# Performance work log

Measured on AMD Instinct MI355X. Metric: run time of the kernel, lower is better.

Reference implementation:

```python
import jax, jax.numpy as jnp
import numpy as np

N_NODES = 100000
N_EDGES = 1600000
IN_CH, HID_CH, OUT_CH = 128, 128, 64


def gcn_conv(x, edge_index, W, b, n_nodes):
    """PyG-style GCNConv: add self-loops, symmetric deg^-1/2 normalization,
    linear transform, scatter-add aggregation, bias."""
    src, dst = edge_index[0], edge_index[1]
    loop = jnp.arange(n_nodes, dtype=src.dtype)
    src = jnp.concatenate([src, loop])
    dst = jnp.concatenate([dst, loop])
    # degree computed on destination side (includes self-loops)
    deg = jax.ops.segment_sum(jnp.ones_like(dst, dtype=x.dtype), dst,
                              num_segments=n_nodes)
    dinv = jnp.where(deg > 0, jax.lax.rsqrt(deg), jnp.zeros_like(deg))
    norm = dinv[src] * dinv[dst]            # [E+N]
    h = x @ W                               # [N, out] transform before aggregate
    msg = h[src] * norm[:, None]            # [E+N, out] gathered+scaled messages
    out = jax.ops.segment_sum(msg, dst, num_segments=n_nodes)
    return out + b


def setup_inputs() -> dict:
    key = jax.random.key(0)
    ks = jax.random.split(key, 6)
    x = jax.random.normal(ks[0], (N_NODES, IN_CH), dtype=jnp.float32)
    pos_edge_index = jax.random.randint(ks[1], (2, N_EDGES), 0, N_NODES, dtype=jnp.int64)
    neg_edge_index = jax.random.randint(ks[2], (2, N_EDGES), 0, N_NODES, dtype=jnp.int64)
    # Glorot-ish init for weights
    W1 = jax.random.normal(ks[3], (IN_CH, HID_CH), dtype=jnp.float32) / np.sqrt(IN_CH)
    b1 = jnp.zeros((HID_CH,), dtype=jnp.float32)
    W2 = jax.random.normal(ks[4], (HID_CH, OUT_CH), dtype=jnp.float32) / np.sqrt(HID_CH)
    b2 = jnp.zeros((OUT_CH,), dtype=jnp.float32)
    return {"x": x, "pos_edge_index": pos_edge_index,
            "neg_edge_index": neg_edge_index,
            "W1": W1, "b1": b1, "W2": W2, "b2": b2}


def reference(x, pos_edge_index, neg_edge_index, W1, b1, W2, b2):
    n = x.shape[0]
    # encode: conv1 -> relu -> conv2 (message passing uses pos_edge_index)
    h = gcn_conv(x, pos_edge_index, W1, b1, n)
    h = jax.nn.relu(h)
    z = gcn_conv(h, pos_edge_index, W2, b2, n)
    # decode: gather node pairs, elementwise mul, sum over feature dim
    pos_pred = jnp.sum(z[pos_edge_index[0]] * z[pos_edge_index[1]], axis=1)
    neg_pred = jnp.sum(z[neg_edge_index[0]] * z[neg_edge_index[1]], axis=1)
    return (pos_pred, neg_pred)
```

## Files before the change

### kernel.cpp

```cpp
#include <hip/hip_runtime.h>


#define IC1 128
#define OC1 128
#define OC2 64

#define BSH    9
#define BNODES (1 << BSH)
#define NBMAX  512
#define CHB    8192
#define CHH    16384

typedef unsigned int u32;
typedef unsigned short u16;
typedef __attribute__((ext_vector_type(8))) short short8v;
typedef __attribute__((ext_vector_type(4))) float f32x4;

__device__ __forceinline__ u16 f2bf(float f) {
  u32 u = __float_as_uint(f);
  u32 r = (u + 0x7fffu + ((u >> 16) & 1u)) >> 16;
  return (u16)r;
}
__device__ __forceinline__ u32 pack2bf(float lo, float hi) {
  return (u32)f2bf(lo) | ((u32)f2bf(hi) << 16);
}
__device__ __forceinline__ float bflo(u32 w) { return __uint_as_float(w << 16); }
__device__ __forceinline__ float bfhi(u32 w) { return __uint_as_float(w & 0xffff0000u); }

__device__ __forceinline__ int getIdx(const void* p, long long i, int is64) {
  return is64 ? (int)((const long long*)p)[i] : ((const int*)p)[i];
}

__global__ void k_detect(const void* pei, long long E, int n_nodes, int* flagbuf,
                         int* bcnt, int NB) {
  __shared__ int bad;
  if (threadIdx.x == 0) bad = 0;
  __syncthreads();
  long long cnt = E < 4096 ? E : 4096;
  const unsigned long long* p64 = (const unsigned long long*)pei;
  for (long long i = threadIdx.x; i < cnt; i += blockDim.x)
    if (p64[i] >= (unsigned long long)n_nodes) bad = 1;
  for (int i = threadIdx.x; i < NB; i += blockDim.x) bcnt[i] = 0;
  __syncthreads();
  if (threadIdx.x == 0) flagbuf[0] = bad ? 0 : 1;
}

__global__ __launch_bounds__(256) void k_hist(const void* pei, long long E,
                                              const int* flagbuf, int* bcnt, int NB) {
  __shared__ int h[NBMAX];
  int f = flagbuf[0];
  for (int i = threadIdx.x; i < NB; i += 256) h[i] = 0;
  __syncthreads();
  long long e0 = (long long)blockIdx.x * CHH;
  long long e1 = min(E, e0 + CHH);
  for (long long e = e0 + threadIdx.x; e < e1; e += 256)
    atomicAdd(&h[getIdx(pei, E + e, f) >> BSH], 1);
  __syncthreads();
  for (int i = threadIdx.x; i < NB; i += 256)
    if (h[i]) atomicAdd(&bcnt[i], h[i]);
}

__global__ __launch_bounds__(256) void k_scan(const int* bcnt, int* boff,
                                              int* gcur, int* rowst, int NB, int N) {
  __shared__ int sa[256];
  __shared__ int carryS;
  if (threadIdx.x == 0) carryS = 0;
  __syncthreads();
  for (int base = 0; base < NB; base += 256) {
    int i = base + threadIdx.x;
    int v = (i < NB) ? bcnt[i] : 0;
    sa[threadIdx.x] = v;
    __syncthreads();
    for (int off = 1; off < 256; off <<= 1) {
      int t = (threadIdx.x >= off) ? sa[threadIdx.x - off] : 0;
      __syncthreads();
      sa[threadIdx.x] += t;
      __syncthreads();
    }
    int exc = sa[threadIdx.x] - v + carryS;
    if (i < NB) { boff[i] = exc; gcur[i] = exc; }
    __syncthreads();
    if (threadIdx.x == 255) carryS += sa[255];
    __syncthreads();
  }
  if (threadIdx.x == 0) { boff[NB] = carryS; rowst[N] = carryS; }
}

__global__ __launch_bounds__(256) void k_bin(const void* pei, long long E,
                                             const int* flagbuf, int* gcur,
                                             u32* binned, int NB) {
  __shared__ u32 stage[CHB];
  __shared__ int h[NBMAX], lofs[NBMAX + 1], cur[NBMAX], gofs[NBMAX];
  __shared__ int sa[256];
  __shared__ int carryS;
  int f = flagbuf[0];
  int tid = threadIdx.x;
  for (int i = tid; i < NB; i += 256) h[i] = 0;
  if (tid == 0) carryS = 0;
  __syncthreads();
  long long e0 = (long long)blockIdx.x * CHB;
  long long e1 = min(E, e0 + CHB);
  int cc = (int)(e1 - e0);
  for (long long e = e0 + tid; e < e1; e += 256)
    atomicAdd(&h[getIdx(pei, E + e, f) >> BSH], 1);
  __syncthreads();
  for (int base = 0; base < NB; base += 256) {
    int i = base + tid;
    int v = (i < NB) ? h[i] : 0;
    sa[tid] = v;
    __syncthreads();
    for (int off = 1; off < 256; off <<= 1) {
      int t = (tid >= off) ? sa[tid - off] : 0;
      __syncthreads();
      sa[tid] += t;
      __syncthreads();
    }
    int exc = sa[tid] - v + carryS;
    if (i < NB) { lofs[i] = exc; cur[i] = exc; }
    __syncthreads();
    if (tid == 255) carryS += sa[255];
    __syncthreads();
  }
  if (tid == 0) lofs[NB] = cc;
  __syncthreads();
  for (long long e = e0 + tid; e < e1; e += 256) {
    int s = getIdx(pei, e, f);
    int d = getIdx(pei, E + e, f);
    int b = d >> BSH;
    int p = atomicAdd(&cur[b], 1);
    stage[p] = (u32)s | ((u32)(d & (BNODES - 1)) << 20);
  }
  __syncthreads();
  for (int b = tid; b < NB; b += 256) {
    int cnt = cur[b] - lofs[b];
    gofs[b] = cnt ? (atomicAdd(&gcur[b], cnt) - lofs[b]) : 0;
  }
  __syncthreads();
  for (int i = tid; i < cc; i += 256) {
    int lo = 0, hi = NB;
    while (hi - lo > 1) {
      int mid = (lo + hi) >> 1;
      if (lofs[mid] <= i) lo = mid; else hi = mid;
    }
    binned[(long long)i + gofs[lo]] = stage[i];
  }
}

__global__ __launch_bounds__(256) void k_fill2(const u32* __restrict__ binned,
                                               const int* __restrict__ boff,
                                               float* __restrict__ dinv,
                                               int* __restrict__ rowst,
                                               u32* __restrict__ csr, int N) {
  __shared__ int cnt[BNODES], sa[BNODES], sb[BNODES], cursor[BNODES];
  int b = blockIdx.x;
  int v0 = b << BSH;
  int nv = min(BNODES, N - v0);
  int tid = threadIdx.x;
  for (int i = tid; i < BNODES; i += 256) cnt[i] = 0;
  __syncthreads();
  int base = boff[b];
  int j1 = boff[b + 1];
  for (int j = base + tid; j < j1; j += 256)
    atomicAdd(&cnt[binned[j] >> 20], 1);
  __syncthreads();
  for (int i = tid; i < BNODES; i += 256) sa[i] = cnt[i];
  __syncthreads();
  int* A = sa; int* B = sb;
  #pragma unroll 1
  for (int off = 1; off < BNODES; off <<= 1) {
    for (int i = tid; i < BNODES; i += 256)
      B[i] = A[i] + ((i >= off) ? A[i - off] : 0);
    __syncthreads();
    int* t = A; A = B; B = t;
  }
  for (int i = tid; i < nv; i += 256) {
    int c = cnt[i];
    int exc = A[i] - c;
    rowst[v0 + i] = base + exc;
    cursor[i] = exc;
    dinv[v0 + i] = rsqrtf((float)(c + 1));
  }
  __syncthreads();
  for (int j = base + tid; j < j1; j += 256) {
    u32 u = binned[j];
    int p = atomicAdd(&cursor[u >> 20], 1);
    csr[base + p] = u & 0xFFFFFu;
  }
}

__global__ void k_prepw(const float* __restrict__ W, u16* __restrict__ Wt,
                        int OC) {
  int i = blockIdx.x * blockDim.x + threadIdx.x;
  if (i >= 128 * OC) return;
  int k = i / OC, c = i % OC;
  Wt[c * 128 + k] = f2bf(W[i]);
}

template<int OC, bool BF16IN>
__global__ __launch_bounds__(256) void k_gemm_mfma(const void* __restrict__ xin,
                                                   const u16* __restrict__ Wt,
                                                   u16* __restrict__ t, int N) {
  constexpr int CT = OC / 16;
  constexpr int LW = 136;
  __shared__ u16 xs[64][LW];
  __shared__ u16 ws[OC][LW];
  const int tid = threadIdx.x;
  const int lane = tid & 63, wv = tid >> 6;
  const long long rowBase = (long long)blockIdx.x * 64;

  if constexpr (BF16IN) {
    const u16* xg = (const u16*)xin;
    #pragma unroll
    for (int i = tid; i < 64 * 16; i += 256) {
      int r = i >> 4, c = i & 15;
      uint4 v = make_uint4(0u, 0u, 0u, 0u);
      if (rowBase + r < N) v = ((const uint4*)(xg + (rowBase + r) * IC1))[c];
      *(uint4*)&xs[r][c * 8] = v;
    }
  } else {
    const float* xg = (const float*)xin;
    #pragma unroll
    for (int i = tid; i < 64 * 16; i += 256) {
      int r = i >> 4, c = i & 15;
      uint4 o = make_uint4(0u, 0u, 0u, 0u);
      if (rowBase + r < N) {
        const float4* src = (const float4*)(xg + (rowBase + r) * IC1 + c * 8);
        float4 a = src[0], bq = src[1];
        o.x = pack2bf(a.x, a.y);  o.y = pack2bf(a.z, a.w);
        o.z = pack2bf(bq.x, bq.y); o.w = pack2bf(bq.z, bq.w);
      }
      *(uint4*)&xs[r][c * 8] = o;
    }
  }
  #pragma unroll
  for (int i = tid; i < OC * 16; i += 256) {
    int r = i >> 4, c = i & 15;
    *(uint4*)&ws[r][c * 8] = ((const uint4*)(Wt + r * 128))[c];
  }
  __syncthreads();

  const int frow = lane & 15, fk = (lane >> 4) * 8;
  short8v a[4];
  #pragma unroll
  for (int kq = 0; kq < 4; ++kq)
    a[kq] = *(const short8v*)&xs[wv * 16 + frow][kq * 32 + fk];

  f32x4 acc[CT];
  #pragma unroll
  for (int ct = 0; ct < CT; ++ct) {
    acc[ct] = (f32x4){0.f, 0.f, 0.f, 0.f};
    #pragma unroll
    for (int kq = 0; kq < 4; ++kq) {
      short8v bfrag = *(const short8v*)&ws[ct * 16 + frow][kq * 32 + fk];
      acc[ct] = __builtin_amdgcn_mfma_f32_16x16x32_bf16(a[kq], bfrag, acc[ct], 0, 0, 0);
    }
  }

  const int crow0 = (lane >> 4) * 4, ccol = lane & 15;
  #pragma unroll
  for (int ct = 0; ct < CT; ++ct) {
    #pragma unroll
    for (int r = 0; r < 4; ++r) {
      long long row = rowBase + wv * 16 + crow0 + r;
      if (row < N) t[row * OC + ct * 16 + ccol] = f2bf(acc[ct][r]);
    }
  }
}

template<int CH>
__global__ __launch_bounds__(256) void k_agg(const u16* __restrict__ t,
                                             u16* __restrict__ out,
                                             const float* __restrict__ dinv,
                                             const int* __restrict__ rowst,
                                             const u32* __restrict__ csr,
                                             const float* __restrict__ bias,
                                             int N, int relu) {
  constexpr int G   = CH / 8;
  constexpr int EPI = 64 / G;
  long long wid = ((long long)blockIdx.x * blockDim.x + threadIdx.x) >> 6;
  int lane = threadIdx.x & 63;
  if (wid >= N) return;
  int v = (int)wid;
  int sub = lane / G;
  int cl  = lane % G;
  float dv = dinv[v];
  float selfw = (sub == 0) ? dv * dv : 0.f;
  float acc[8];
  {
    uint4 u = ((const uint4*)(t + (long long)v * CH))[cl];
    acc[0] = bflo(u.x) * selfw; acc[1] = bfhi(u.x) * selfw;
    acc[2] = bflo(u.y) * selfw; acc[3] = bfhi(u.y) * selfw;
    acc[4] = bflo(u.z) * selfw; acc[5] = bfhi(u.z) * selfw;
    acc[6] = bflo(u.w) * selfw; acc[7] = bfhi(u.w) * selfw;
  }
  int st = rowst[v];
  int cnt = rowst[v + 1] - st;
  for (int base = 0; base < cnt; base += 64) {
    int m = min(64, cnt - base);
    int s = 0; float w = 0.f;
    if (lane < m) { s = (int)csr[st + base + lane]; w = dinv[s] * dv; }
    int iters = (m + EPI - 1) / EPI;
    #pragma unroll 2
    for (int j = 0; j < iters; ++j) {
      int src  = __shfl(s, j * EPI + sub);
      float ww = __shfl(w, j * EPI + sub);
      uint4 u = ((const uint4*)(t + (long long)src * CH))[cl];
      acc[0] += bflo(u.x) * ww; acc[1] += bfhi(u.x) * ww;
      acc[2] += bflo(u.y) * ww; acc[3] += bfhi(u.y) * ww;
      acc[4] += bflo(u.z) * ww; acc[5] += bfhi(u.z) * ww;
      acc[6] += bflo(u.w) * ww; acc[7] += bfhi(u.w) * ww;
    }
  }
  #pragma unroll
  for (int off = G; off < 64; off <<= 1) {
    #pragma unroll
    for (int i = 0; i < 8; ++i) acc[i] += __shfl_xor(acc[i], off);
  }
  if (sub == 0) {
    float4 b0 = ((const float4*)bias)[cl * 2];
    float4 b1 = ((const float4*)bias)[cl * 2 + 1];
    float o[8] = {acc[0] + b0.x, acc[1] + b0.y, acc[2] + b0.z, acc[3] + b0.w,
                  acc[4] + b1.x, acc[5] + b1.y, acc[6] + b1.z, acc[7] + b1.w};
    if (relu) {
      #pragma unroll
      for (int i = 0; i < 8; ++i) o[i] = fmaxf(o[i], 0.f);
    }
    uint4 w4;
    w4.x = pack2bf(o[0], o[1]); w4.y = pack2bf(o[2], o[3]);
    w4.z = pack2bf(o[4], o[5]); w4.w = pack2bf(o[6], o[7]);
    ((uint4*)(out + (long long)v * CH))[cl] = w4;
  }
}

__global__ __launch_bounds__(256) void k_decode(const u16* __restrict__ z,
                                                const void* pei, const void* nei,
                                                float* __restrict__ out,
                                                long long E, const int* flagbuf) {
  int f = flagbuf[0];
  long long g = ((long long)blockIdx.x * blockDim.x + threadIdx.x) >> 3;
  int wi = threadIdx.x & 7;
  if (g >= 2 * E) return;
  const void* ei = (g < E) ? pei : nei;
  long long e = (g < E) ? g : g - E;
  int s = getIdx(ei, e, f);
  int d = getIdx(ei, E + e, f);
  uint4 a = ((const uint4*)(z + (long long)s * OC2))[wi];
  uint4 b = ((const uint4*)(z + (long long)d * OC2))[wi];
  float p = bflo(a.x) * bflo(b.x) + bfhi(a.x) * bfhi(b.x)
          + bflo(a.y) * bflo(b.y) + bfhi(a.y) * bfhi(b.y)
          + bflo(a.z) * bflo(b.z) + bfhi(a.z) * bfhi(b.z)
          + bflo(a.w) * bflo(b.w) + bfhi(a.w) * bfhi(b.w);
  p += __shfl_xor(p, 4);
  p += __shfl_xor(p, 2);
  p += __shfl_xor(p, 1);
  if (wi == 0) out[g] = p;
}

extern "C" void kernel_launch(void* const* d_in, const int* in_sizes, int n_in,
                              void* d_out, int out_size, void* d_ws, size_t ws_size,
                              hipStream_t stream) {
  const float* x  = (const float*)d_in[0];
  const void*  pei = d_in[1];
  const void*  nei = d_in[2];
  const float* W1 = (const float*)d_in[3];
  const float* b1 = (const float*)d_in[4];
  const float* W2 = (const float*)d_in[5];
  const float* b2 = (const float*)d_in[6];
  float* out = (float*)d_out;

  const int       N  = in_sizes[0] / IC1;
  const long long E  = in_sizes[1] / 2;
  const int       NB = (N + BNODES - 1) >> BSH;

  char* p = (char*)d_ws;
  auto carve = [&](size_t bytes) { char* r = p; p += ((bytes + 255) & ~(size_t)255); return r; };
  int*   flagbuf = (int*)  carve(8);
  float* dinv    = (float*)carve((size_t)N * 4);
  int*   rowst   = (int*)  carve((size_t)(N + 1) * 4);
  int*   bcnt    = (int*)  carve((size_t)NB * 4);
  int*   boff    = (int*)  carve((size_t)(NB + 1) * 4);
  int*   gcur    = (int*)  carve((size_t)NB * 4);
  u32*   binned  = (u32*)  carve((size_t)E * 4);
  u32*   csr     = (u32*)  carve((size_t)E * 4);
  u16*   Wt      = (u16*)  carve((size_t)128 * 128 * 2);
  u16*   bufA    = (u16*)  carve((size_t)N * IC1 * 2);
  u16*   bufB    = (u16*)  carve((size_t)N * IC1 * 2);

  const int B = 256;

  k_detect<<<1, B, 0, stream>>>(pei, E, N, flagbuf, bcnt, NB);
  k_hist<<<dim3((unsigned)((E + CHH - 1) / CHH)), B, 0, stream>>>(pei, E, flagbuf,
                                                                  bcnt, NB);
  k_scan<<<1, B, 0, stream>>>(bcnt, boff, gcur, rowst, NB, N);
  k_bin<<<dim3((unsigned)((E + CHB - 1) / CHB)), B, 0, stream>>>(pei, E, flagbuf,
                                                                 gcur, binned, NB);
  k_fill2<<<dim3(NB), B, 0, stream>>>(binned, boff, dinv, rowst, csr, N);

  k_prepw<<<dim3((128 * OC1 + B - 1) / B), B, 0, stream>>>(W1, Wt, OC1);
  k_gemm_mfma<OC1, false><<<dim3((N + 63) / 64), B, 0, stream>>>(x, Wt, bufA, N);
  k_agg<OC1><<<dim3((N + 3) / 4), B, 0, stream>>>(bufA, bufB, dinv, rowst,
                                                  csr, b1, N, 1);

  k_prepw<<<dim3((128 * OC2 + B - 1) / B), B, 0, stream>>>(W2, Wt, OC2);
  k_gemm_mfma<OC2, true><<<dim3((N + 63) / 64), B, 0, stream>>>(bufB, Wt, bufA, N);
  k_agg<OC2><<<dim3((N + 3) / 4), B, 0, stream>>>(bufA, bufB, dinv, rowst,
                                                  csr, b2, N, 0);

  long long groups = 2 * E;
  dim3 gD((unsigned)((groups * 8 + B - 1) / B));
  k_decode<<<gD, B, 0, stream>>>(bufB, pei, nei, out, E, flagbuf);
}
```

Before: 444.1 us.

## Fold scan into bin/fill kernels, merge weight prep, enlarge GEMM row tiles

Removes the single-block k_scan launch: each k_bin block now recomputes the global bucket prefix from bcnt, and each k_fill2 block sums the preceding bucket counts itself to find its base offset. Weight conversion for both layers is merged into one k_prepw launch. The GEMM now processes 128 rows per block, reads B fragments directly from global instead of staging them in LDS, and reuses each B fragment for two row tiles. It also halves the edge chunk sizes, moves k_fill2 to 512 threads, and unrolls the aggregation loop further. The tradeoff is redundant prefix work in every block and uncached global reads of the weight fragments.

```diff
diff --git a/kernel.cpp b/kernel.cpp
--- a/kernel.cpp
+++ b/kernel.cpp
@@ -8,8 +8,8 @@
 #define BSH    9
 #define BNODES (1 << BSH)
 #define NBMAX  512
-#define CHB    8192
-#define CHH    16384
+#define CHB    4096
+#define CHH    4096
 
 typedef unsigned int u32;
 typedef unsigned short u16;
@@ -32,7 +32,7 @@
 }
 
 __global__ void k_detect(const void* pei, long long E, int n_nodes, int* flagbuf,
-                         int* bcnt, int NB) {
+                         int* bcnt, int* gcur0, int NB) {
   __shared__ int bad;
   if (threadIdx.x == 0) bad = 0;
   __syncthreads();
@@ -40,7 +40,7 @@
   const unsigned long long* p64 = (const unsigned long long*)pei;
   for (long long i = threadIdx.x; i < cnt; i += blockDim.x)
     if (p64[i] >= (unsigned long long)n_nodes) bad = 1;
-  for (int i = threadIdx.x; i < NB; i += blockDim.x) bcnt[i] = 0;
+  for (int i = threadIdx.x; i < NB; i += blockDim.x) { bcnt[i] = 0; gcur0[i] = 0; }
   __syncthreads();
   if (threadIdx.x == 0) flagbuf[0] = bad ? 0 : 1;
 }
@@ -60,37 +60,11 @@
     if (h[i]) atomicAdd(&bcnt[i], h[i]);
 }
 
-__global__ __launch_bounds__(256) void k_scan(const int* bcnt, int* boff,
-                                              int* gcur, int* rowst, int NB, int N) {
-  __shared__ int sa[256];
-  __shared__ int carryS;
-  if (threadIdx.x == 0) carryS = 0;
-  __syncthreads();
-  for (int base = 0; base < NB; base += 256) {
-    int i = base + threadIdx.x;
-    int v = (i < NB) ? bcnt[i] : 0;
-    sa[threadIdx.x] = v;
-    __syncthreads();
-    for (int off = 1; off < 256; off <<= 1) {
-      int t = (threadIdx.x >= off) ? sa[threadIdx.x - off] : 0;
-      __syncthreads();
-      sa[threadIdx.x] += t;
-      __syncthreads();
-    }
-    int exc = sa[threadIdx.x] - v + carryS;
-    if (i < NB) { boff[i] = exc; gcur[i] = exc; }
-    __syncthreads();
-    if (threadIdx.x == 255) carryS += sa[255];
-    __syncthreads();
-  }
-  if (threadIdx.x == 0) { boff[NB] = carryS; rowst[N] = carryS; }
-}
-
 __global__ __launch_bounds__(256) void k_bin(const void* pei, long long E,
-                                             const int* flagbuf, int* gcur,
-                                             u32* binned, int NB) {
+                                             const int* flagbuf, const int* bcnt,
+                                             int* gcur0, u32* binned, int NB) {
   __shared__ u32 stage[CHB];
-  __shared__ int h[NBMAX], lofs[NBMAX + 1], cur[NBMAX], gofs[NBMAX];
+  __shared__ int h[NBMAX], lofs[NBMAX + 1], cur[NBMAX], gofs[NBMAX], gboff[NBMAX];
   __shared__ int sa[256];
   __shared__ int carryS;
   int f = flagbuf[0];
@@ -121,8 +95,25 @@
     if (tid == 255) carryS += sa[255];
     __syncthreads();
   }
-  if (tid == 0) lofs[NB] = cc;
-  __syncthreads();
+  if (tid == 0) { lofs[NB] = cc; carryS = 0; }
+  __syncthreads();
+  for (int base = 0; base < NB; base += 256) {
+    int i = base + tid;
+    int v = (i < NB) ? bcnt[i] : 0;
+    sa[tid] = v;
+    __syncthreads();
+    for (int off = 1; off < 256; off <<= 1) {
+      int t = (tid >= off) ? sa[tid - off] : 0;
+      __syncthreads();
+      sa[tid] += t;
+      __syncthreads();
+    }
+    int exc = sa[tid] - v + carryS;
+    if (i < NB) gboff[i] = exc;
+    __syncthreads();
+    if (tid == 255) carryS += sa[255];
+    __syncthreads();
+  }
   for (long long e = e0 + tid; e < e1; e += 256) {
     int s = getIdx(pei, e, f);
     int d = getIdx(pei, E + e, f);
@@ -133,7 +124,7 @@
   __syncthreads();
   for (int b = tid; b < NB; b += 256) {
     int cnt = cur[b] - lofs[b];
-    gofs[b] = cnt ? (atomicAdd(&gcur[b], cnt) - lofs[b]) : 0;
+    gofs[b] = cnt ? (gboff[b] + atomicAdd(&gcur0[b], cnt) - lofs[b]) : 0;
   }
   __syncthreads();
   for (int i = tid; i < cc; i += 256) {
@@ -146,54 +137,75 @@
   }
 }
 
-__global__ __launch_bounds__(256) void k_fill2(const u32* __restrict__ binned,
-                                               const int* __restrict__ boff,
+__global__ __launch_bounds__(512) void k_fill2(const u32* __restrict__ binned,
+                                               const int* __restrict__ bcnt,
                                                float* __restrict__ dinv,
                                                int* __restrict__ rowst,
-                                               u32* __restrict__ csr, int N) {
+                                               u32* __restrict__ csr, int N, int NB) {
   __shared__ int cnt[BNODES], sa[BNODES], sb[BNODES], cursor[BNODES];
+  __shared__ int redu[8];
+  __shared__ int baseS;
   int b = blockIdx.x;
   int v0 = b << BSH;
   int nv = min(BNODES, N - v0);
   int tid = threadIdx.x;
-  for (int i = tid; i < BNODES; i += 256) cnt[i] = 0;
-  __syncthreads();
-  int base = boff[b];
-  int j1 = boff[b + 1];
-  for (int j = base + tid; j < j1; j += 256)
+  int part = 0;
+  for (int i = tid; i < b; i += 512) part += bcnt[i];
+  #pragma unroll
+  for (int off = 32; off; off >>= 1) part += __shfl_down(part, off);
+  if ((tid & 63) == 0) redu[tid >> 6] = part;
+  for (int i = tid; i < BNODES; i += 512) cnt[i] = 0;
+  __syncthreads();
+  if (tid == 0) {
+    int s = 0;
+    #pragma unroll
+    for (int w = 0; w < 8; ++w) s += redu[w];
+    baseS = s;
+  }
+  __syncthreads();
+  int base = baseS;
+  int j1 = base + bcnt[b];
+  for (int j = base + tid; j < j1; j += 512)
     atomicAdd(&cnt[binned[j] >> 20], 1);
   __syncthreads();
-  for (int i = tid; i < BNODES; i += 256) sa[i] = cnt[i];
+  sa[tid] = cnt[tid];
   __syncthreads();
   int* A = sa; int* B = sb;
   #pragma unroll 1
   for (int off = 1; off < BNODES; off <<= 1) {
-    for (int i = tid; i < BNODES; i += 256)
-      B[i] = A[i] + ((i >= off) ? A[i - off] : 0);
+    B[tid] = A[tid] + ((tid >= off) ? A[tid - off] : 0);
     __syncthreads();
     int* t = A; A = B; B = t;
   }
-  for (int i = tid; i < nv; i += 256) {
-    int c = cnt[i];
-    int exc = A[i] - c;
-    rowst[v0 + i] = base + exc;
-    cursor[i] = exc;
-    dinv[v0 + i] = rsqrtf((float)(c + 1));
-  }
-  __syncthreads();
-  for (int j = base + tid; j < j1; j += 256) {
+  if (tid < nv) {
+    int c = cnt[tid];
+    int exc = A[tid] - c;
+    rowst[v0 + tid] = base + exc;
+    cursor[tid] = exc;
+    dinv[v0 + tid] = rsqrtf((float)(c + 1));
+  }
+  if (b == NB - 1 && tid == 0) rowst[N] = j1;
+  __syncthreads();
+  for (int j = base + tid; j < j1; j += 512) {
     u32 u = binned[j];
     int p = atomicAdd(&cursor[u >> 20], 1);
     csr[base + p] = u & 0xFFFFFu;
   }
 }
 
-__global__ void k_prepw(const float* __restrict__ W, u16* __restrict__ Wt,
-                        int OC) {
+__global__ void k_prepw(const float* __restrict__ W1, const float* __restrict__ W2,
+                        u16* __restrict__ Wt1, u16* __restrict__ Wt2) {
   int i = blockIdx.x * blockDim.x + threadIdx.x;
-  if (i >= 128 * OC) return;
-  int k = i / OC, c = i % OC;
-  Wt[c * 128 + k] = f2bf(W[i]);
+  if (i < 128 * OC1) {
+    int k = i / OC1, c = i % OC1;
+    Wt1[c * 128 + k] = f2bf(W1[i]);
+  } else {
+    int j = i - 128 * OC1;
+    if (j < 128 * OC2) {
+      int k = j / OC2, c = j % OC2;
+      Wt2[c * 128 + k] = f2bf(W2[j]);
+    }
+  }
 }
 
 template<int OC, bool BF16IN>
@@ -202,16 +214,15 @@
                                                    u16* __restrict__ t, int N) {
   constexpr int CT = OC / 16;
   constexpr int LW = 136;
-  __shared__ u16 xs[64][LW];
-  __shared__ u16 ws[OC][LW];
+  __shared__ u16 xs[128][LW];
   const int tid = threadIdx.x;
   const int lane = tid & 63, wv = tid >> 6;
-  const long long rowBase = (long long)blockIdx.x * 64;
+  const long long rowBase = (long long)blockIdx.x * 128;
 
   if constexpr (BF16IN) {
     const u16* xg = (const u16*)xin;
     #pragma unroll
-    for (int i = tid; i < 64 * 16; i += 256) {
+    for (int i = tid; i < 128 * 16; i += 256) {
       int r = i >> 4, c = i & 15;
       uint4 v = make_uint4(0u, 0u, 0u, 0u);
       if (rowBase + r < N) v = ((const uint4*)(xg + (rowBase + r) * IC1))[c];
@@ -220,7 +231,7 @@
   } else {
     const float* xg = (const float*)xin;
     #pragma unroll
-    for (int i = tid; i < 64 * 16; i += 256) {
+    for (int i = tid; i < 128 * 16; i += 256) {
       int r = i >> 4, c = i & 15;
       uint4 o = make_uint4(0u, 0u, 0u, 0u);
       if (rowBase + r < N) {
@@ -232,39 +243,39 @@
       *(uint4*)&xs[r][c * 8] = o;
     }
   }
+  __syncthreads();
+
+  const int frow = lane & 15, fk = (lane >> 4) * 8;
+  short8v a[2][4];
   #pragma unroll
-  for (int i = tid; i < OC * 16; i += 256) {
-    int r = i >> 4, c = i & 15;
-    *(uint4*)&ws[r][c * 8] = ((const uint4*)(Wt + r * 128))[c];
-  }
-  __syncthreads();
-
-  const int frow = lane & 15, fk = (lane >> 4) * 8;
-  short8v a[4];
-  #pragma unroll
-  for (int kq = 0; kq < 4; ++kq)
-    a[kq] = *(const short8v*)&xs[wv * 16 + frow][kq * 32 + fk];
-
-  f32x4 acc[CT];
+  for (int rt = 0; rt < 2; ++rt)
+    #pragma unroll
+    for (int kq = 0; kq < 4; ++kq)
+      a[rt][kq] = *(const short8v*)&xs[wv * 32 + rt * 16 + frow][kq * 32 + fk];
+
+  f32x4 acc[2][CT];
   #pragma unroll
   for (int ct = 0; ct < CT; ++ct) {
-    acc[ct] = (f32x4){0.f, 0.f, 0.f, 0.f};
+    acc[0][ct] = (f32x4){0.f, 0.f, 0.f, 0.f};
+    acc[1][ct] = (f32x4){0.f, 0.f, 0.f, 0.f};
     #pragma unroll
     for (int kq = 0; kq < 4; ++kq) {
-      short8v bfrag = *(const short8v*)&ws[ct * 16 + frow][kq * 32 + fk];
-      acc[ct] = __builtin_amdgcn_mfma_f32_16x16x32_bf16(a[kq], bfrag, acc[ct], 0, 0, 0);
+      short8v bfrag = *(const short8v*)(Wt + (ct * 16 + frow) * 128 + kq * 32 + fk);
+      acc[0][ct] = __builtin_amdgcn_mfma_f32_16x16x32_bf16(a[0][kq], bfrag, acc[0][ct], 0, 0, 0);
+      acc[1][ct] = __builtin_amdgcn_mfma_f32_16x16x32_bf16(a[1][kq], bfrag, acc[1][ct], 0, 0, 0);
     }
   }
 
   const int crow0 = (lane >> 4) * 4, ccol = lane & 15;
   #pragma unroll
-  for (int ct = 0; ct < CT; ++ct) {
-    #pragma unroll
-    for (int r = 0; r < 4; ++r) {
-      long long row = rowBase + wv * 16 + crow0 + r;
-      if (row < N) t[row * OC + ct * 16 + ccol] = f2bf(acc[ct][r]);
-    }
-  }
+  for (int rt = 0; rt < 2; ++rt)
+    #pragma unroll
+    for (int ct = 0; ct < CT; ++ct)
+      #pragma unroll
+      for (int r = 0; r < 4; ++r) {
+        long long row = rowBase + wv * 32 + rt * 16 + crow0 + r;
+        if (row < N) t[row * OC + ct * 16 + ccol] = f2bf(acc[rt][ct][r]);
+      }
 }
 
 template<int CH>
@@ -300,7 +311,7 @@
     int s = 0; float w = 0.f;
     if (lane < m) { s = (int)csr[st + base + lane]; w = dinv[s] * dv; }
     int iters = (m + EPI - 1) / EPI;
-    #pragma unroll 2
+    #pragma unroll 4
     for (int j = 0; j < iters; ++j) {
       int src  = __shfl(s, j * EPI + sub);
       float ww = __shfl(w, j * EPI + sub);
@@ -378,31 +389,31 @@
   float* dinv    = (float*)carve((size_t)N * 4);
   int*   rowst   = (int*)  carve((size_t)(N + 1) * 4);
   int*   bcnt    = (int*)  carve((size_t)NB * 4);
-  int*   boff    = (int*)  carve((size_t)(NB + 1) * 4);
-  int*   gcur    = (int*)  carve((size_t)NB * 4);
+  int*   gcur0   = (int*)  carve((size_t)NB * 4);
   u32*   binned  = (u32*)  carve((size_t)E * 4);
   u32*   csr     = (u32*)  carve((size_t)E * 4);
-  u16*   Wt      = (u16*)  carve((size_t)128 * 128 * 2);
+  u16*   Wt1     = (u16*)  carve((size_t)128 * OC1 * 2);
+  u16*   Wt2     = (u16*)  carve((size_t)128 * OC2 * 2);
   u16*   bufA    = (u16*)  carve((size_t)N * IC1 * 2);
   u16*   bufB    = (u16*)  carve((size_t)N * IC1 * 2);
 
   const int B = 256;
 
-  k_detect<<<1, B, 0, stream>>>(pei, E, N, flagbuf, bcnt, NB);
+  k_detect<<<1, B, 0, stream>>>(pei, E, N, flagbuf, bcnt, gcur0, NB);
   k_hist<<<dim3((unsigned)((E + CHH - 1) / CHH)), B, 0, stream>>>(pei, E, flagbuf,
                                                                   bcnt, NB);
-  k_scan<<<1, B, 0, stream>>>(bcnt, boff, gcur, rowst, NB, N);
   k_bin<<<dim3((unsigned)((E + CHB - 1) / CHB)), B, 0, stream>>>(pei, E, flagbuf,
-                                                                 gcur, binned, NB);
-  k_fill2<<<dim3(NB), B, 0, stream>>>(binned, boff, dinv, rowst, csr, N);
-
-  k_prepw<<<dim3((128 * OC1 + B - 1) / B), B, 0, stream>>>(W1, Wt, OC1);
-  k_gemm_mfma<OC1, false><<<dim3((N + 63) / 64), B, 0, stream>>>(x, Wt, bufA, N);
+                                                                 bcnt, gcur0,
+                                                                 binned, NB);
+  k_fill2<<<dim3(NB), 512, 0, stream>>>(binned, bcnt, dinv, rowst, csr, N, NB);
+
+  k_prepw<<<dim3((128 * (OC1 + OC2) + B - 1) / B), B, 0, stream>>>(W1, W2, Wt1, Wt2);
+
+  k_gemm_mfma<OC1, false><<<dim3((N + 127) / 128), B, 0, stream>>>(x, Wt1, bufA, N);
   k_agg<OC1><<<dim3((N + 3) / 4), B, 0, stream>>>(bufA, bufB, dinv, rowst,
                                                   csr, b1, N, 1);
 
-  k_prepw<<<dim3((128 * OC2 + B - 1) / B), B, 0, stream>>>(W2, Wt, OC2);
-  k_gemm_mfma<OC2, true><<<dim3((N + 63) / 64), B, 0, stream>>>(bufB, Wt, bufA, N);
+  k_gemm_mfma<OC2, true><<<dim3((N + 127) / 128), B, 0, stream>>>(bufB, Wt2, bufA, N);
   k_agg<OC2><<<dim3((N + 3) / 4), B, 0, stream>>>(bufA, bufB, dinv, rowst,
                                                   csr, b2, N, 0);
 
```

Result: faster. 412.7 us (-7.1%).
